# Performance work log

Measured on AMD Instinct MI355X. Metric: run time of the kernel, lower is better.

## Reference

```python
import jax, jax.numpy as jnp
import numpy as np

INPUT_SIZE = 2048
HIDDEN_SIZE = 4096
NUM_CLASSES = 1000
BATCH = 4096


def setup_inputs() -> dict:
    key = jax.random.key(0)
    kx, k1, k2, k3 = jax.random.split(key, 4)
    x = jax.random.normal(kx, (BATCH, INPUT_SIZE), dtype=jnp.float32)
    w1 = jax.random.normal(k1, (INPUT_SIZE, HIDDEN_SIZE), dtype=jnp.float32) * 0.01
    b1 = jnp.zeros((HIDDEN_SIZE,), dtype=jnp.float32)
    w2 = jax.random.normal(k2, (HIDDEN_SIZE, HIDDEN_SIZE), dtype=jnp.float32) * 0.01
    b2 = jnp.zeros((HIDDEN_SIZE,), dtype=jnp.float32)
    w3 = jax.random.normal(k3, (HIDDEN_SIZE, NUM_CLASSES), dtype=jnp.float32) * 0.01
    b3 = jnp.zeros((NUM_CLASSES,), dtype=jnp.float32)
    return {"x": x, "w1": w1, "b1": b1, "w2": w2, "b2": b2, "w3": w3, "b3": b3}


def reference(x, w1, b1, w2, b2, w3, b3):
    # fused GEMM + bias + ReLU, equivalent to the original Python double-loop matmul
    h1 = jax.nn.relu(x @ w1 + b1)    # [B, H]
    h2 = jax.nn.relu(h1 @ w2 + b2)   # [B, H]
    out = h2 @ w3 + b3               # [B, C]
    return out
```

## Files before the change

kernel.cpp:

```cpp
#include <hip/hip_runtime.h>
#include <hip/hip_bf16.h>

typedef __bf16 bf16x8 __attribute__((ext_vector_type(8)));
typedef __bf16 bf16x4 __attribute__((ext_vector_type(4)));
typedef float floatx4 __attribute__((ext_vector_type(4)));

#define B_    4096
#define IN_   2048
#define HID_  4096
#define NC_   1000
#define NCP_  1024

__device__ __forceinline__ void transpose_cvt_dev(const float* __restrict__ src,
                                                  __bf16* __restrict__ dst,
                                                  int R, int C, int bx, int by,
                                                  float* tile ) {
    const int r0 = bx * 64;
    const int c0 = by * 64;
    const int t  = threadIdx.x;
#pragma unroll
    for (int it = 0; it < 4; ++it) {
        int lin = it * 256 + t;
        int sr = lin >> 4, c4 = lin & 15;
        int cb = c0 + c4 * 4;
        const float* s = src + (size_t)(r0 + sr) * C;
        float4 v;
        if (cb + 3 < C) {
            v = *(const float4*)(s + cb);
        } else {
            v.x = (cb + 0 < C) ? s[cb + 0] : 0.f;
            v.y = (cb + 1 < C) ? s[cb + 1] : 0.f;
            v.z = (cb + 2 < C) ? s[cb + 2] : 0.f;
            v.w = (cb + 3 < C) ? s[cb + 3] : 0.f;
        }
        tile[(c4 * 4 + 0) * 65 + sr] = v.x;
        tile[(c4 * 4 + 1) * 65 + sr] = v.y;
        tile[(c4 * 4 + 2) * 65 + sr] = v.z;
        tile[(c4 * 4 + 3) * 65 + sr] = v.w;
    }
    __syncthreads();
#pragma unroll
    for (int it = 0; it < 2; ++it) {
        int lin = it * 256 + t;
        int dr = lin >> 3, q8 = lin & 7;
        bf16x8 o;
#pragma unroll
        for (int j = 0; j < 8; ++j) o[j] = (__bf16)tile[dr * 65 + q8 * 8 + j];
        *(bf16x8*)(dst + (size_t)(c0 + dr) * R + r0 + q8 * 8) = o;
    }
}

__device__ __forceinline__ void swizzle32x32(int bid, int& bx, int& by) {
    int xcd = bid & 7;
    int q   = bid >> 3;
    by = ((xcd >> 2) << 4) + (q & 15);
    bx = ((xcd & 3) << 3) + (q >> 4);
}

template <bool RELU, bool OUT_BF16>
__device__ __forceinline__ void gemm_core(const __bf16* __restrict__ A,
                                          const __bf16* __restrict__ Bt,
                                          const float* __restrict__ bias,
                                          void* __restrict__ Cv,
                                          int M, int K, int Nstore,
                                          int bx, int by,
                                          __bf16* sA, __bf16* sB) {
    const int tid   = threadIdx.x;
    const int lane  = tid & 63;
    const int wave  = tid >> 6;
    const int wr    = wave >> 1;
    const int wc    = wave & 1;
    const int mBase = by * 128;
    const int nBase = bx * 128;
    const int lr    = lane >> 4;
    const int lc    = lane & 15;

    floatx4 acc[4][4];
#pragma unroll
    for (int i = 0; i < 4; ++i)
#pragma unroll
        for (int j = 0; j < 4; ++j) acc[i][j] = (floatx4)0.f;

    for (int k0 = 0; k0 < K; k0 += 64) {
#pragma unroll
        for (int it = 0; it < 4; ++it) {
            int lin = it * 256 + tid;
            int r   = lin >> 3;
            int kc  = (lin & 7) ^ (r & 7);
            const __bf16* ga = A  + (size_t)(mBase + r) * K + k0 + kc * 8;
            const __bf16* gb = Bt + (size_t)(nBase + r) * K + k0 + kc * 8;
            __builtin_amdgcn_global_load_lds(
                (__attribute__((address_space(1))) void*)ga,
                (__attribute__((address_space(3))) void*)(sA + lin * 8), 16, 0, 0);
            __builtin_amdgcn_global_load_lds(
                (__attribute__((address_space(1))) void*)gb,
                (__attribute__((address_space(3))) void*)(sB + lin * 8), 16, 0, 0);
        }
        __builtin_amdgcn_s_waitcnt(0);
        __syncthreads();

#pragma unroll
        for (int kk = 0; kk < 2; ++kk) {
            const int sw = (kk * 4 + lr) ^ (lc & 7);
            bf16x8 af[4], bfr[4];
#pragma unroll
            for (int i = 0; i < 4; ++i)
                af[i] = *(const bf16x8*)(sA + (wr * 64 + i * 16 + lc) * 64 + sw * 8);
#pragma unroll
            for (int j = 0; j < 4; ++j)
                bfr[j] = *(const bf16x8*)(sB + (wc * 64 + j * 16 + lc) * 64 + sw * 8);
#pragma unroll
            for (int i = 0; i < 4; ++i)
#pragma unroll
                for (int j = 0; j < 4; ++j)
                    acc[i][j] = __builtin_amdgcn_mfma_f32_16x16x32_bf16(af[i], bfr[j], acc[i][j], 0, 0, 0);
        }
        __syncthreads();
    }

#pragma unroll
    for (int j = 0; j < 4; ++j) {
        int col = nBase + wc * 64 + j * 16 + lc;
        if (col < Nstore) {
            float bv = bias[col];
#pragma unroll
            for (int i = 0; i < 4; ++i) {
                int rowb = mBase + wr * 64 + i * 16 + lr * 4;
#pragma unroll
                for (int r = 0; r < 4; ++r) {
                    float v = acc[i][j][r] + bv;
                    if (RELU) v = fmaxf(v, 0.f);
                    if (OUT_BF16)
                        ((__bf16*)Cv)[(size_t)(rowb + r) * Nstore + col] = (__bf16)v;
                    else
                        ((float*)Cv)[(size_t)(rowb + r) * Nstore + col] = v;
                }
            }
        }
    }
}

__global__ __launch_bounds__(256) void prep1(const float* __restrict__ x,
                                             __bf16* __restrict__ xb,
                                             const float* __restrict__ w1,
                                             __bf16* __restrict__ w1t) {
    __shared__ float tile[64 * 65];
    const int b = blockIdx.x;
    if (b < 4096) {
        int i = (b * 256 + (int)threadIdx.x) * 8;
        float4 a = *(const float4*)(x + i);
        float4 c = *(const float4*)(x + i + 4);
        bf16x8 o;
        o[0] = (__bf16)a.x; o[1] = (__bf16)a.y; o[2] = (__bf16)a.z; o[3] = (__bf16)a.w;
        o[4] = (__bf16)c.x; o[5] = (__bf16)c.y; o[6] = (__bf16)c.z; o[7] = (__bf16)c.w;
        *(bf16x8*)(xb + i) = o;
    } else {
        int l = b - 4096;
        transpose_cvt_dev(w1, w1t, IN_, HID_, l & 31, l >> 5, tile);
    }
}

__global__ __launch_bounds__(256, 2) void gemm1_fused(const __bf16* __restrict__ xb,
                                                      const __bf16* __restrict__ w1t,
                                                      const float* __restrict__ b1,
                                                      __bf16* __restrict__ h1,
                                                      const float* __restrict__ w2,
                                                      __bf16* __restrict__ w2t,
                                                      const float* __restrict__ w3,
                                                      __bf16* __restrict__ w3t) {
    __shared__ float smem[8192];
    const int b = blockIdx.x;
    if (b < 1024) {
        __bf16* sA = (__bf16*)smem;
        __bf16* sB = sA + 128 * 64;
        int bx, by;
        swizzle32x32(b, bx, by);
        gemm_core<true, true>(xb, w1t, b1, h1, B_, IN_, HID_, bx, by, sA, sB);
    } else if (b < 5120) {
        int l = b - 1024;
        transpose_cvt_dev(w2, w2t, HID_, HID_, l & 63, l >> 6, smem);
    } else {
        int l = b - 5120;
        transpose_cvt_dev(w3, w3t, HID_, NC_, l & 63, l >> 6, smem);
    }
}

#define PRIO1 __builtin_amdgcn_s_setprio(1)
#define PRIO0 __builtin_amdgcn_s_setprio(0)
#define BAR() __builtin_amdgcn_s_barrier()
#define LGKM(n)                                                  \
    asm volatile("s_waitcnt lgkmcnt(" #n ")" ::: "memory");      \
    __builtin_amdgcn_sched_barrier(0)
#define VMCNT(n) asm volatile("s_waitcnt vmcnt(" #n ")" ::: "memory")

#define LDA2(dst, mb, pA)                                                      \
    _Pragma("unroll") for (int mi_ = 0; mi_ < 2; ++mi_)                        \
    _Pragma("unroll") for (int kk_ = 0; kk_ < 2; ++kk_)                        \
        dst[mi_][kk_] = *(const bf16x8*)((pA) +                                \
            (wr * 128 + ((mb) + mi_) * 16 + lc) * 64 +                         \
            (((kk_ * 4) + lr) ^ (lc & 7)) * 8);

#define LDB8(pB)                                                               \
    _Pragma("unroll") for (int n_ = 0; n_ < 4; ++n_)                           \
    _Pragma("unroll") for (int kk_ = 0; kk_ < 2; ++kk_)                        \
        bq[n_][kk_] = *(const bf16x8*)((pB) +                                  \
            (wc * 64 + n_ * 16 + lc) * 64 +                                    \
            (((kk_ * 4) + lr) ^ (lc & 7)) * 8);

#define MFMA16(aset, mb)                                                       \
    _Pragma("unroll") for (int mi_ = 0; mi_ < 2; ++mi_)                        \
    _Pragma("unroll") for (int n_ = 0; n_ < 4; ++n_) {                         \
        acc[(mb) + mi_][n_] = __builtin_amdgcn_mfma_f32_16x16x32_bf16(         \
            aset[mi_][0], bq[n_][0], acc[(mb) + mi_][n_], 0, 0, 0);            \
        acc[(mb) + mi_][n_] = __builtin_amdgcn_mfma_f32_16x16x32_bf16(         \
            aset[mi_][1], bq[n_][1], acc[(mb) + mi_][n_], 0, 0, 0);            \
    }

#define STAGE4(kt, base)                                                       \
    stage_half(A,  mBase,       (kt) * 64, (base));                            \
    stage_half(A,  mBase + 128, (kt) * 64, (base) + 8192);                     \
    stage_half(Bt, nBase,       (kt) * 64, (base) + 16384);                    \
    stage_half(Bt, nBase + 128, (kt) * 64, (base) + 24576);

#define TILE_S(CUR, OTH, ktS) {                                                \
    VMCNT(0);                        \
    BAR();                                         \
    const __bf16* pA_ = (CUR);                                                 \
    const __bf16* pB_ = (CUR) + 16384;                                         \
    bf16x8 bq[4][2], aX[2][2], aY[2][2];                                       \
    LDB8(pB_); LDA2(aX, 0, pA_); LDA2(aY, 2, pA_);            \
    STAGE4(ktS, OTH);                   \
    LGKM(4);                                                                   \
    PRIO1; MFMA16(aX, 0); PRIO0; BAR();                                        \
    LDA2(aX, 4, pA_);                                                          \
    BAR(); LGKM(4); PRIO1; MFMA16(aY, 2); PRIO0; BAR();                        \
    LDA2(aY, 6, pA_);                                                          \
    BAR(); LGKM(4); PRIO1; MFMA16(aX, 4); PRIO0; BAR();                        \
    LGKM(0); PRIO1; MFMA16(aY, 6); PRIO0; BAR();      \
}

#define TILE_L(CUR) {                                                          \
    VMCNT(0);                                                                  \
    BAR();                                                                     \
    const __bf16* pA_ = (CUR);                                                 \
    const __bf16* pB_ = (CUR) + 16384;                                         \
    bf16x8 bq[4][2], aX[2][2], aY[2][2];                                       \
    LDB8(pB_); LDA2(aX, 0, pA_); LDA2(aY, 2, pA_);                             \
    LGKM(4);                                                                   \
    PRIO1; MFMA16(aX, 0); PRIO0; BAR();                                        \
    LDA2(aX, 4, pA_);                                                          \
    BAR(); LGKM(4); PRIO1; MFMA16(aY, 2); PRIO0; BAR();                        \
    LDA2(aY, 6, pA_);                                                          \
    BAR(); LGKM(4); PRIO1; MFMA16(aX, 4); PRIO0; BAR();                        \
    LGKM(0); MFMA16(aY, 6);                                                    \
}

__global__ __launch_bounds__(512, 1) void gemm2_256(const __bf16* __restrict__ A,
                                                    const __bf16* __restrict__ Bt,
                                                    const float* __restrict__ bias,
                                                    __bf16* __restrict__ C) {
    extern __shared__ __bf16 lds[];
    const int tid  = threadIdx.x;
    const int lane = tid & 63;
    const int wave = tid >> 6;
    const int wr   = wave >> 2;
    const int wc   = wave & 3;
    const int lr   = lane >> 4;
    const int lc   = lane & 15;

    int bid = blockIdx.y * 16 + blockIdx.x;
    int xcd = bid & 7, q = bid >> 3;
    const int by = (xcd & 3) * 4 + (q & 3);
    const int bx = (xcd >> 2) * 8 + (q >> 2);
    const int mBase = by * 256;
    const int nBase = bx * 256;

    __bf16* const S0p = lds;
    __bf16* const S1p = lds + 32768;

    auto stage_half = [&](const __bf16* __restrict__ src, int rowBase, int k0,
                          __bf16* dst) {
#pragma unroll
        for (int it = 0; it < 2; ++it) {
            int lin = it * 512 + tid;
            int rl  = lin >> 3;
            int kc  = (lin & 7) ^ (rl & 7);
            const __bf16* gp = src + (size_t)(rowBase + rl) * HID_ + k0 + kc * 8;
            __builtin_amdgcn_global_load_lds(
                (__attribute__((address_space(1))) void*)gp,
                (__attribute__((address_space(3))) void*)(dst + lin * 8), 16, 0, 0);
        }
    };

    floatx4 acc[8][4];
#pragma unroll
    for (int i = 0; i < 8; ++i)
#pragma unroll
        for (int j = 0; j < 4; ++j) acc[i][j] = (floatx4)0.f;

    STAGE4(0, S0p);

    for (int t = 0; t < 62; t += 2) {
        TILE_S(S0p, S1p, t + 1);
        TILE_S(S1p, S0p, t + 2);
    }
    TILE_S(S0p, S1p, 63);
    TILE_L(S1p);

#pragma unroll
    for (int n = 0; n < 4; ++n) {
        int col = nBase + wc * 64 + n * 16 + lc;
        float bv = bias[col];
#pragma unroll
        for (int m = 0; m < 8; ++m) {
            int rowb = mBase + wr * 128 + m * 16 + lr * 4;
#pragma unroll
            for (int r = 0; r < 4; ++r) {
                float v = fmaxf(acc[m][n][r] + bv, 0.f);
                C[(size_t)(rowb + r) * HID_ + col] = (__bf16)v;
            }
        }
    }
}

__global__ __launch_bounds__(256, 2) void gemm_sk(const __bf16* __restrict__ A,
                                                  const __bf16* __restrict__ Bt,
                                                  float* __restrict__ P,
                                                  int M, int KH, int Ktot) {
    __shared__ __bf16 sA[128 * 64];
    __shared__ __bf16 sB[128 * 64];

    const int tid   = threadIdx.x;
    const int lane  = tid & 63;
    const int wave  = tid >> 6;
    const int wr    = wave >> 1;
    const int wc    = wave & 1;
    const int mBase = blockIdx.y * 128;
    const int nBase = blockIdx.x * 128;
    const int z     = blockIdx.z;
    const int kOff  = z * KH;
    const int lr    = lane >> 4;
    const int lc    = lane & 15;

    floatx4 acc[4][4];
#pragma unroll
    for (int i = 0; i < 4; ++i)
#pragma unroll
        for (int j = 0; j < 4; ++j) acc[i][j] = (floatx4)0.f;

    for (int k0 = kOff; k0 < kOff + KH; k0 += 64) {
#pragma unroll
        for (int it = 0; it < 4; ++it) {
            int lin = it * 256 + tid;
            int r   = lin >> 3;
            int kc  = (lin & 7) ^ (r & 7);
            const __bf16* ga = A  + (size_t)(mBase + r) * Ktot + k0 + kc * 8;
            const __bf16* gb = Bt + (size_t)(nBase + r) * Ktot + k0 + kc * 8;
            __builtin_amdgcn_global_load_lds(
                (__attribute__((address_space(1))) void*)ga,
                (__attribute__((address_space(3))) void*)(sA + lin * 8), 16, 0, 0);
            __builtin_amdgcn_global_load_lds(
                (__attribute__((address_space(1))) void*)gb,
                (__attribute__((address_space(3))) void*)(sB + lin * 8), 16, 0, 0);
        }
        __builtin_amdgcn_s_waitcnt(0);
        __syncthreads();

#pragma unroll
        for (int kk = 0; kk < 2; ++kk) {
            const int sw = (kk * 4 + lr) ^ (lc & 7);
            bf16x8 af[4], bfr[4];
#pragma unroll
            for (int i = 0; i < 4; ++i)
                af[i] = *(const bf16x8*)(sA + (wr * 64 + i * 16 + lc) * 64 + sw * 8);
#pragma unroll
            for (int j = 0; j < 4; ++j)
                bfr[j] = *(const bf16x8*)(sB + (wc * 64 + j * 16 + lc) * 64 + sw * 8);
#pragma unroll
            for (int i = 0; i < 4; ++i)
#pragma unroll
                for (int j = 0; j < 4; ++j)
                    acc[i][j] = __builtin_amdgcn_mfma_f32_16x16x32_bf16(af[i], bfr[j], acc[i][j], 0, 0, 0);
        }
        __syncthreads();
    }

    float* Pz = P + (size_t)z * M * NCP_;
#pragma unroll
    for (int j = 0; j < 4; ++j) {
        int col = nBase + wc * 64 + j * 16 + lc;
#pragma unroll
        for (int i = 0; i < 4; ++i) {
            int rowb = mBase + wr * 64 + i * 16 + lr * 4;
#pragma unroll
            for (int r = 0; r < 4; ++r)
                Pz[(size_t)(rowb + r) * NCP_ + col] = acc[i][j][r];
        }
    }
}

__global__ __launch_bounds__(256) void reduce_bias(const float* __restrict__ P,
                                                   const float* __restrict__ b3,
                                                   float* __restrict__ out) {
    int c = blockIdx.x * 256 + threadIdx.x;
    int m = blockIdx.y;
    if (c < NC_)
        out[(size_t)m * NC_ + c] =
            P[(size_t)m * NCP_ + c] + P[(size_t)(B_ + m) * NCP_ + c] + b3[c];
}

extern "C" void kernel_launch(void* const* d_in, const int* in_sizes, int n_in,
                              void* d_out, int out_size, void* d_ws, size_t ws_size,
                              hipStream_t stream) {
    const float* x  = (const float*)d_in[0];
    const float* w1 = (const float*)d_in[1];
    const float* b1 = (const float*)d_in[2];
    const float* w2 = (const float*)d_in[3];
    const float* b2 = (const float*)d_in[4];
    const float* w3 = (const float*)d_in[5];
    const float* b3 = (const float*)d_in[6];
    float* out = (float*)d_out;

    char* ws = (char*)d_ws;
    __bf16* xb  = (__bf16*)(ws);
    __bf16* w1t = (__bf16*)(ws + (16u << 20));
    __bf16* w2t = (__bf16*)(ws + (32u << 20));
    __bf16* w3t = (__bf16*)(ws + (64u << 20));
    __bf16* h1  = (__bf16*)(ws + (72u << 20));
    __bf16* h2  = (__bf16*)(ws);
    float*  P   = (float*)(ws + (72u << 20));

    static int attr_done = 0;
    if (!attr_done) {
        (void)hipFuncSetAttribute((const void*)gemm2_256,
                                  hipFuncAttributeMaxDynamicSharedMemorySize,
                                  131072);
        attr_done = 1;
    }

    prep1<<<6144, 256, 0, stream>>>(x, xb, w1, w1t);

    gemm1_fused<<<6144, 256, 0, stream>>>(xb, w1t, b1, h1, w2, w2t, w3, w3t);

    gemm2_256<<<dim3(16, 16), 512, 131072, stream>>>(h1, w2t, b2, h2);

    gemm_sk<<<dim3(NCP_ / 128, B_ / 128, 2), 256, 0, stream>>>(
        h2, w3t, P, B_, HID_ / 2, HID_);
    reduce_bias<<<dim3(NCP_ / 256, B_), 256, 0, stream>>>(P, b3, out);
}
```

Measured before the change: 424.7 us.

## Prefetch next tile's LDS fragments during final MFMA phase of gemm2

Restructures the double-buffered main loop of the 256x256 hidden-layer GEMM so the B fragments and first A fragments of the next K-tile are read from LDS while the last MFMA group of the current tile runs. It also moves the global-to-LDS staging to the start of each tile and defers the vmcnt wait to later in the tile. The aim is to hide LDS read latency and the barrier at tile boundaries behind matrix-core work. In exchange it adds register pressure and relies on careful barrier and waitcnt placement to avoid reading an LDS buffer while it is being overwritten.

```diff
diff --git a/kernel.cpp b/kernel.cpp
--- a/kernel.cpp
+++ b/kernel.cpp
@@ -188,6 +188,7 @@
 #define PRIO1 __builtin_amdgcn_s_setprio(1)
 #define PRIO0 __builtin_amdgcn_s_setprio(0)
 #define BAR() __builtin_amdgcn_s_barrier()
+#define SB0 __builtin_amdgcn_sched_barrier(0)
 #define LGKM(n)                                                  \
     asm volatile("s_waitcnt lgkmcnt(" #n ")" ::: "memory");      \
     __builtin_amdgcn_sched_barrier(0)
@@ -200,12 +201,25 @@
             (wr * 128 + ((mb) + mi_) * 16 + lc) * 64 +                         \
             (((kk_ * 4) + lr) ^ (lc & 7)) * 8);
 
-#define LDB8(pB)                                                               \
-    _Pragma("unroll") for (int n_ = 0; n_ < 4; ++n_)                           \
+#define RDB2(np, base)                                                         \
+    _Pragma("unroll") for (int j_ = 0; j_ < 2; ++j_)                           \
     _Pragma("unroll") for (int kk_ = 0; kk_ < 2; ++kk_)                        \
-        bq[n_][kk_] = *(const bf16x8*)((pB) +                                  \
-            (wc * 64 + n_ * 16 + lc) * 64 +                                    \
+        bq[(np) * 2 + j_][kk_] = *(const bf16x8*)((base) + 16384 +             \
+            (wc * 64 + ((np) * 2 + j_) * 16 + lc) * 64 +                       \
             (((kk_ * 4) + lr) ^ (lc & 7)) * 8);
+
+#define MFMA8(aset, mb, np)                                                    \
+    _Pragma("unroll") for (int mi_ = 0; mi_ < 2; ++mi_)                        \
+    _Pragma("unroll") for (int j_ = 0; j_ < 2; ++j_) {                         \
+        acc[(mb) + mi_][(np) * 2 + j_] =                                       \
+            __builtin_amdgcn_mfma_f32_16x16x32_bf16(                           \
+                aset[mi_][0], bq[(np) * 2 + j_][0],                            \
+                acc[(mb) + mi_][(np) * 2 + j_], 0, 0, 0);                      \
+        acc[(mb) + mi_][(np) * 2 + j_] =                                       \
+            __builtin_amdgcn_mfma_f32_16x16x32_bf16(                           \
+                aset[mi_][1], bq[(np) * 2 + j_][1],                            \
+                acc[(mb) + mi_][(np) * 2 + j_], 0, 0, 0);                      \
+    }
 
 #define MFMA16(aset, mb)                                                       \
     _Pragma("unroll") for (int mi_ = 0; mi_ < 2; ++mi_)                        \
@@ -222,37 +236,48 @@
     stage_half(Bt, nBase,       (kt) * 64, (base) + 16384);                    \
     stage_half(Bt, nBase + 128, (kt) * 64, (base) + 24576);
 
-#define TILE_S(CUR, OTH, ktS) {                                                \
-    VMCNT(0);                        \
+#define TILE3(CUR, NXT, ktS) {                                                 \
+                                                                       \
+    STAGE4(ktS, NXT);                                                          \
+    LDA2(aY, 2, CUR); SB0;                   \
+    LGKM(8);                                                \
+    PRIO1; MFMA8(aX, 0, 0); PRIO0;                                             \
+    LGKM(4);                                      \
+    PRIO1; MFMA8(aX, 0, 1); PRIO0;                                             \
+    BAR();                                                                     \
+                                                                       \
+    LDA2(aX, 4, CUR); SB0;                                        \
+    LGKM(4);                                                     \
+    PRIO1; MFMA16(aY, 2); PRIO0;                                               \
+    BAR();                                                                     \
+                                                                       \
+    LDA2(aY, 6, CUR); SB0;                                        \
+    VMCNT(0);                             \
+    LGKM(4);                                                     \
+    PRIO1; MFMA16(aX, 4); PRIO0;                                               \
     BAR();                                         \
-    const __bf16* pA_ = (CUR);                                                 \
-    const __bf16* pB_ = (CUR) + 16384;                                         \
-    bf16x8 bq[4][2], aX[2][2], aY[2][2];                                       \
-    LDB8(pB_); LDA2(aX, 0, pA_); LDA2(aY, 2, pA_);            \
-    STAGE4(ktS, OTH);                   \
-    LGKM(4);                                                                   \
-    PRIO1; MFMA16(aX, 0); PRIO0; BAR();                                        \
-    LDA2(aX, 4, pA_);                                                          \
-    BAR(); LGKM(4); PRIO1; MFMA16(aY, 2); PRIO0; BAR();                        \
-    LDA2(aY, 6, pA_);                                                          \
-    BAR(); LGKM(4); PRIO1; MFMA16(aX, 4); PRIO0; BAR();                        \
-    LGKM(0); PRIO1; MFMA16(aY, 6); PRIO0; BAR();      \
-}
-
-#define TILE_L(CUR) {                                                          \
-    VMCNT(0);                                                                  \
+                                                                       \
+    LGKM(0);                                                     \
+    PRIO1; MFMA8(aY, 6, 0); PRIO0; SB0;                         \
+    RDB2(0, NXT); SB0;                                   \
+    PRIO1; MFMA8(aY, 6, 1); PRIO0; SB0;                     \
+    LDA2(aX, 0, NXT);                                  \
+    RDB2(1, NXT); SB0;                                       \
+    BAR();                                                    \
+}
+
+#define TILE_LAST(CUR) {                                                       \
+    LDA2(aY, 2, CUR); SB0;                                                     \
+    LGKM(8); PRIO1; MFMA8(aX, 0, 0); PRIO0;                                    \
+    LGKM(4); PRIO1; MFMA8(aX, 0, 1); PRIO0;                                    \
     BAR();                                                                     \
-    const __bf16* pA_ = (CUR);                                                 \
-    const __bf16* pB_ = (CUR) + 16384;                                         \
-    bf16x8 bq[4][2], aX[2][2], aY[2][2];                                       \
-    LDB8(pB_); LDA2(aX, 0, pA_); LDA2(aY, 2, pA_);                             \
-    LGKM(4);                                                                   \
-    PRIO1; MFMA16(aX, 0); PRIO0; BAR();                                        \
-    LDA2(aX, 4, pA_);                                                          \
-    BAR(); LGKM(4); PRIO1; MFMA16(aY, 2); PRIO0; BAR();                        \
-    LDA2(aY, 6, pA_);                                                          \
-    BAR(); LGKM(4); PRIO1; MFMA16(aX, 4); PRIO0; BAR();                        \
-    LGKM(0); MFMA16(aY, 6);                                                    \
+    LDA2(aX, 4, CUR); SB0;                                                     \
+    LGKM(4); PRIO1; MFMA16(aY, 2); PRIO0;                                      \
+    BAR();                                                                     \
+    LDA2(aY, 6, CUR); SB0;                                                     \
+    LGKM(4); PRIO1; MFMA16(aX, 4); PRIO0;                                      \
+    BAR();                                                                     \
+    LGKM(0); MFMA8(aY, 6, 0); MFMA8(aY, 6, 1);                                 \
 }
 
 __global__ __launch_bounds__(512, 1) void gemm2_256(const __bf16* __restrict__ A,
@@ -298,14 +323,22 @@
 #pragma unroll
         for (int j = 0; j < 4; ++j) acc[i][j] = (floatx4)0.f;
 
+    bf16x8 bq[4][2];
+    bf16x8 aX[2][2], aY[2][2];
+
     STAGE4(0, S0p);
+    VMCNT(0);
+    BAR();
+    RDB2(0, S0p); SB0;
+    LDA2(aX, 0, S0p); SB0;
+    RDB2(1, S0p); SB0;
 
     for (int t = 0; t < 62; t += 2) {
-        TILE_S(S0p, S1p, t + 1);
-        TILE_S(S1p, S0p, t + 2);
-    }
-    TILE_S(S0p, S1p, 63);
-    TILE_L(S1p);
+        TILE3(S0p, S1p, t + 1);
+        TILE3(S1p, S0p, t + 2);
+    }
+    TILE3(S0p, S1p, 63);
+    TILE_LAST(S1p);
 
 #pragma unroll
     for (int n = 0; n < 4; ++n) {
```

Result: slower. 474.5 us (+11.7%).
